# Kernel tuning notes

Measured on AMD Instinct MI355X. Metric: run time of the kernel, lower is better.

Reference implementation:

```python
import jax, jax.numpy as jnp
import numpy as np

B, C, T = 64, 128, 4096
KNOT = 4  # default knot=4 -> 6 spline knots
SIGMA = 0.2


def setup_inputs() -> dict:
    key = jax.random.key(0)
    k1, k2, k3 = jax.random.split(key, 3)
    x = jax.random.normal(k1, (B, C, T), dtype=jnp.float32)
    # yy ~ N(1.0, sigma) as in GenerateRandomCurves
    yy = 1.0 + SIGMA * jax.random.normal(k2, (B, KNOT + 2, C), dtype=jnp.float32)
    mask_rand = jax.random.uniform(k3, (B, 1, 1), dtype=jnp.float32)
    return {"x": x, "yy": yy, "mask_rand": mask_rand}


def _notaknot_matrix(n, h):
    # Moment (second-derivative) system for a not-a-knot cubic spline on a
    # uniform grid with spacing h (matches scipy.interpolate.CubicSpline default bc).
    A = np.zeros((n, n), dtype=np.float32)
    for i in range(1, n - 1):
        A[i, i - 1] = h / 6.0
        A[i, i] = 2.0 * h / 3.0
        A[i, i + 1] = h / 6.0
    # not-a-knot: third derivative continuous at x1 and x_{n-2}
    A[0, 0], A[0, 1], A[0, 2] = 1.0, -2.0, 1.0
    A[-1, -3], A[-1, -2], A[-1, -1] = 1.0, -2.0, 1.0
    return jnp.asarray(A)


def reference(x, yy, mask_rand):
    Bq, Cq, Tq = x.shape
    n = KNOT + 2
    h = (Tq - 1) / (KNOT + 1)  # uniform knot spacing; knots span [0, T-1]
    A = _notaknot_matrix(n, h)

    # Solve for spline moments M (second derivatives at knots), batched over (B, C).
    rhs_int = (yy[:, 2:, :] - 2.0 * yy[:, 1:-1, :] + yy[:, :-2, :]) / h  # (B, n-2, C)
    z = jnp.zeros((Bq, 1, Cq), yy.dtype)
    rhs = jnp.concatenate([z, rhs_int, z], axis=1)  # (B, n, C)
    M = jnp.linalg.solve(A, rhs)  # (B, n, C)

    # Evaluate the spline at t = 0..T-1 (vectorized over all batch/channel).
    tq = jnp.arange(Tq, dtype=x.dtype)
    idx = jnp.clip(jnp.floor(tq / h).astype(jnp.int32), 0, n - 2)  # (T,)
    xl = idx.astype(x.dtype) * h
    dxl = (tq - xl)[None, :, None]       # t - x_i
    dxr = (xl + h - tq)[None, :, None]   # x_{i+1} - t
    Mi, Mi1 = M[:, idx, :], M[:, idx + 1, :]      # (B, T, C)
    yi, yi1 = yy[:, idx, :], yy[:, idx + 1, :]    # (B, T, C)
    curve = ((Mi * dxr**3 + Mi1 * dxl**3) / (6.0 * h)
             + (yi / h - Mi * h / 6.0) * dxr
             + (yi1 / h - Mi1 * h / 6.0) * dxl)   # (B, T, C)

    # DistortTimesteps: cumulative sum, rescaled so the last step lands on T-1.
    tt = jnp.cumsum(curve, axis=1)
    tt = tt * (Tq - 1) / tt[:, -1:, :]  # (B, T, C)

    # Per-(batch, channel) linear interpolation back onto the regular grid.
    xp = tt.transpose(0, 2, 1).reshape(Bq * Cq, Tq)  # warped timestamps
    fp = x.reshape(Bq * Cq, Tq)                      # channel signals
    x_tw = jax.vmap(lambda a, b: jnp.interp(tq, a, b))(xp, fp)
    x_tw = x_tw.reshape(Bq, Cq, Tq)

    mask = mask_rand < 0.5  # (B,1,1): apply warp with probability p=0.5
    return jnp.where(mask, x_tw, x)
```

## Files before the change

kernel.cpp:

```cpp
#include <hip/hip_runtime.h>

#define BB 64
#define CC 128
#define TT 4096
#define NN 6
#define HH 819.0f
#define NTHR 512
#define EPT 8
#define NWAVE (NTHR / 64)
#define NROW (BB * CC)
#define NSPAN 5
#define TABBYTES ((size_t)NROW * NSPAN * 16)

typedef float f4 __attribute__((ext_vector_type(4)));

__device__ __forceinline__ void nt_store4(float* p, f4 v) {
    __builtin_nontemporal_store(v, (f4*)p);
}

__device__ __forceinline__ int padi(int j) { return j + (j >> 5); }

__device__ __forceinline__ void spline_solve(const float* __restrict__ yy,
                                             int b, int c, float* y, float* Mv)
{
    #pragma unroll
    for (int k = 0; k < NN; ++k)
        y[k] = yy[((size_t)b * NN + k) * CC + c];
    float Aug[NN][NN + 1];
    #pragma unroll
    for (int i = 0; i < NN; ++i)
        #pragma unroll
        for (int j = 0; j < NN + 1; ++j)
            Aug[i][j] = 0.0f;
    Aug[0][0] = 1.0f;  Aug[0][1] = -2.0f;  Aug[0][2] = 1.0f;
    Aug[5][3] = 1.0f;  Aug[5][4] = -2.0f;  Aug[5][5] = 1.0f;
    #pragma unroll
    for (int i = 1; i < NN - 1; ++i) {
        Aug[i][i - 1] = HH / 6.0f;
        Aug[i][i]     = 2.0f * HH / 3.0f;
        Aug[i][i + 1] = HH / 6.0f;
        Aug[i][NN]    = (y[i + 1] - 2.0f * y[i] + y[i - 1]) / HH;
    }
    #pragma unroll
    for (int k = 0; k < NN; ++k) {
        float inv = 1.0f / Aug[k][k];
        #pragma unroll
        for (int i = k + 1; i < NN; ++i) {
            float m = Aug[i][k] * inv;
            #pragma unroll
            for (int j = k; j < NN + 1; ++j)
                Aug[i][j] -= m * Aug[k][j];
        }
    }
    #pragma unroll
    for (int i = NN - 1; i >= 0; --i) {
        float s = Aug[i][NN];
        #pragma unroll
        for (int j = i + 1; j < NN; ++j)
            s -= Aug[i][j] * Mv[j];
        Mv[i] = s / Aug[i][i];
    }
}

__global__ __launch_bounds__(256) void spline_coef_kernel(
    const float* __restrict__ yy, f4* __restrict__ tab)
{
    const int row = blockIdx.x * 256 + threadIdx.x;
    const int b = row / CC;
    const int c = row % CC;
    float y[NN], Mv[NN];
    spline_solve(yy, b, c, y, Mv);
    const float invh  = 1.0f / HH;
    const float inv6h = 1.0f / (6.0f * HH);
    #pragma unroll
    for (int s = 0; s < NSPAN; ++s) {
        f4 cf;
        cf.x = y[s];
        cf.y = (y[s + 1] - y[s]) * invh - Mv[s] * (HH / 3.0f) - Mv[s + 1] * (HH / 6.0f);
        cf.z = Mv[s] * 0.5f;
        cf.w = (Mv[s + 1] - Mv[s]) * inv6h;
        tab[row * NSPAN + s] = cf;
    }
}

template <int TABLE>
__global__ __launch_bounds__(NTHR) void timewarp_kernel(
    const float* __restrict__ x,
    const float* __restrict__ yy,
    const float* __restrict__ mask_rand,
    const f4* __restrict__ tab,
    float* __restrict__ out)
{
    const int row = blockIdx.x;
    const int b   = row / CC;
    const int tid = threadIdx.x;

    const float* xrow = x + (size_t)row * TT;
    float* orow       = out + (size_t)row * TT;

    if (!(mask_rand[b] < 0.5f)) {
        const f4* xi = (const f4*)xrow;
        nt_store4(orow + 4 * tid,          xi[tid]);
        nt_store4(orow + 4 * (tid + NTHR), xi[tid + NTHR]);
        return;
    }

    __shared__ float sh_res[TT + TT / 32];
    __shared__ float sh_xx[NTHR];
    __shared__ float sh_wsum[NWAVE];

    const int t0 = tid * EPT;
    int idxA = t0 / 819;  if (idxA > 4) idxA = 4;
    int idxB = idxA + 1;  if (idxB > 4) idxB = 4;

    const f4 v0 = *(const f4*)(xrow + t0);
    const f4 v1 = *(const f4*)(xrow + t0 + 4);
    const float fpb = xrow[(t0 + EPT < TT) ? (t0 + EPT) : (TT - 1)];

    f4 cfA, cfB;
    if (TABLE) {
        cfA = tab[row * NSPAN + idxA];
        cfB = tab[row * NSPAN + idxB];
    } else {
        const int c = row % CC;
        float y[NN], Mv[NN];
        spline_solve(yy, b, c, y, Mv);
        const float invh  = 1.0f / HH;
        const float inv6h = 1.0f / (6.0f * HH);
        float MiA = Mv[0], Mi1A = Mv[1], yiA = y[0], yi1A = y[1];
        #pragma unroll
        for (int s = 1; s <= 4; ++s)
            if (idxA >= s) { MiA = Mv[s]; Mi1A = Mv[s + 1]; yiA = y[s]; yi1A = y[s + 1]; }
        float MiB = Mv[0], Mi1B = Mv[1], yiB = y[0], yi1B = y[1];
        #pragma unroll
        for (int s = 1; s <= 4; ++s)
            if (idxB >= s) { MiB = Mv[s]; Mi1B = Mv[s + 1]; yiB = y[s]; yi1B = y[s + 1]; }
        cfA.x = yiA;
        cfA.y = (yi1A - yiA) * invh - MiA * (HH / 3.0f) - Mi1A * (HH / 6.0f);
        cfA.z = MiA * 0.5f;
        cfA.w = (Mi1A - MiA) * inv6h;
        cfB.x = yiB;
        cfB.y = (yi1B - yiB) * invh - MiB * (HH / 3.0f) - Mi1B * (HH / 6.0f);
        cfB.z = MiB * 0.5f;
        cfB.w = (Mi1B - MiB) * inv6h;
    }

    float fpv[EPT];
    fpv[0] = v0.x; fpv[1] = v0.y; fpv[2] = v0.z; fpv[3] = v0.w;
    fpv[4] = v1.x; fpv[5] = v1.y; fpv[6] = v1.z; fpv[7] = v1.w;

    const float xlA = (float)idxA * HH;
    const float xlB = (float)idxB * HH;
    const float tb  = (float)((idxA + 1) * 819);

    float loc[EPT];
    float running = 0.0f;
    #pragma unroll
    for (int k = 0; k < EPT; ++k) {
        float ft = (float)(t0 + k);
        bool inB = ft >= tb;
        f4    cf = inB ? cfB : cfA;
        float xl = inB ? xlB : xlA;
        float s  = ft - xl;
        running += fmaf(s, fmaf(s, fmaf(s, cf.w, cf.z), cf.y), cf.x);
        loc[k] = running;
    }

    const int lane = tid & 63, wid = tid >> 6;
    float ws = running;
    #pragma unroll
    for (int d = 1; d < 64; d <<= 1) {
        float v = __shfl_up(ws, d, 64);
        if (lane >= d) ws += v;
    }
    if (lane == 63) sh_wsum[wid] = ws;
    __syncthreads();
    float wo = 0.0f, total = 0.0f;
    #pragma unroll
    for (int w = 0; w < NWAVE; ++w) {
        float s = sh_wsum[w];
        total += s;
        if (w < wid) wo += s;
    }
    const float offs  = wo + (ws - running);
    const float scale = 4095.0f / total;

    float xpv[EPT + 1];
    #pragma unroll
    for (int k = 0; k < EPT; ++k)
        xpv[k] = (loc[k] + offs) * scale;
    sh_xx[tid] = xpv[0];
    __syncthreads();
    xpv[EPT] = (tid < NTHR - 1) ? sh_xx[tid + 1] : 4095.0f;

    #pragma unroll
    for (int k = 0; k < EPT; ++k) {
        const int seg = t0 + k;
        if (seg < TT - 1) {
            float xa = xpv[k], xb = xpv[k + 1];
            float fa = fpv[k];
            float fb = (k < EPT - 1) ? fpv[k + 1] : fpb;
            float d  = xb - xa;
            float slope = (d > 0.0f) ? (fb - fa) * __builtin_amdgcn_rcpf(d) : 0.0f;
            float a0 = fmaf(-xa, slope, fa);
            int qlo = (int)ceilf(xa);  if (qlo < 0) qlo = 0;
            int qhi = (int)ceilf(xb);  if (qhi > TT) qhi = TT;
            for (int q = qlo; q < qhi; ++q)
                sh_res[padi(q)] = fmaf((float)q, slope, a0);
        }
    }
    if (tid == 0) {
        int q1 = (int)ceilf(xpv[0]);  if (q1 > TT) q1 = TT;
        for (int q = 0; q < q1; ++q) sh_res[padi(q)] = fpv[0];
    }
    if (tid == NTHR - 1) {
        int q0 = (int)ceilf(xpv[EPT - 1]);  if (q0 < 0) q0 = 0;
        for (int q = q0; q < TT; ++q) sh_res[padi(q)] = fpv[EPT - 1];
    }
    __syncthreads();

    #pragma unroll
    for (int kk = 0; kk < 2; ++kk) {
        int i4 = tid + NTHR * kk;
        int fb4 = 4 * i4;
        int p  = padi(fb4);
        f4 v;
        v.x = sh_res[p + 0];
        v.y = sh_res[p + 1];
        v.z = sh_res[p + 2];
        v.w = sh_res[p + 3];
        nt_store4(orow + fb4, v);
    }
}

extern "C" void kernel_launch(void* const* d_in, const int* in_sizes, int n_in,
                              void* d_out, int out_size, void* d_ws, size_t ws_size,
                              hipStream_t stream) {
    const float* x    = (const float*)d_in[0];
    const float* yy   = (const float*)d_in[1];
    const float* mask = (const float*)d_in[2];
    float* out = (float*)d_out;

    if (d_ws != nullptr && ws_size >= TABBYTES) {
        f4* tab = (f4*)d_ws;
        spline_coef_kernel<<<dim3(NROW / 256), dim3(256), 0, stream>>>(yy, tab);
        timewarp_kernel<1><<<dim3(NROW), dim3(NTHR), 0, stream>>>(x, yy, mask, tab, out);
    } else {
        timewarp_kernel<0><<<dim3(NROW), dim3(NTHR), 0, stream>>>(x, yy, mask, nullptr, out);
    }
}
```

Baseline: 235.4 us.

## Process two rows per block and replace shared-memory neighbor exchange with shuffle

```diff
diff --git a/kernel.cpp b/kernel.cpp
--- a/kernel.cpp
+++ b/kernel.cpp
@@ -11,6 +11,7 @@
 #define NROW (BB * CC)
 #define NSPAN 5
 #define TABBYTES ((size_t)NROW * NSPAN * 16)
+#define PADSZ (TT + TT / 32)
 
 typedef float f4 __attribute__((ext_vector_type(4)));
 
@@ -62,6 +63,22 @@
     }
 }
 
+__device__ __forceinline__ void horner_coefs(const float* y, const float* Mv,
+                                             f4* out5)
+{
+    const float invh  = 1.0f / HH;
+    const float inv6h = 1.0f / (6.0f * HH);
+    #pragma unroll
+    for (int s = 0; s < NSPAN; ++s) {
+        f4 cf;
+        cf.x = y[s];
+        cf.y = (y[s + 1] - y[s]) * invh - Mv[s] * (HH / 3.0f) - Mv[s + 1] * (HH / 6.0f);
+        cf.z = Mv[s] * 0.5f;
+        cf.w = (Mv[s + 1] - Mv[s]) * inv6h;
+        out5[s] = cf;
+    }
+}
+
 __global__ __launch_bounds__(256) void spline_coef_kernel(
     const float* __restrict__ yy, f4* __restrict__ tab)
 {
@@ -70,17 +87,11 @@
     const int c = row % CC;
     float y[NN], Mv[NN];
     spline_solve(yy, b, c, y, Mv);
-    const float invh  = 1.0f / HH;
-    const float inv6h = 1.0f / (6.0f * HH);
-    #pragma unroll
-    for (int s = 0; s < NSPAN; ++s) {
-        f4 cf;
-        cf.x = y[s];
-        cf.y = (y[s + 1] - y[s]) * invh - Mv[s] * (HH / 3.0f) - Mv[s + 1] * (HH / 6.0f);
-        cf.z = Mv[s] * 0.5f;
-        cf.w = (Mv[s + 1] - Mv[s]) * inv6h;
-        tab[row * NSPAN + s] = cf;
-    }
+    f4 cf[NSPAN];
+    horner_coefs(y, Mv, cf);
+    #pragma unroll
+    for (int s = 0; s < NSPAN; ++s)
+        tab[row * NSPAN + s] = cf[s];
 }
 
 template <int TABLE>
@@ -91,145 +102,189 @@
     const f4* __restrict__ tab,
     float* __restrict__ out)
 {
-    const int row = blockIdx.x;
-    const int b   = row / CC;
+    const int r0  = 2 * blockIdx.x;
+    const int r1  = r0 + 1;
+    const int b   = r0 / CC;
     const int tid = threadIdx.x;
 
-    const float* xrow = x + (size_t)row * TT;
-    float* orow       = out + (size_t)row * TT;
+    const float* xr0 = x + (size_t)r0 * TT;
+    const float* xr1 = x + (size_t)r1 * TT;
+    float* or0       = out + (size_t)r0 * TT;
+    float* or1       = out + (size_t)r1 * TT;
 
     if (!(mask_rand[b] < 0.5f)) {
-        const f4* xi = (const f4*)xrow;
-        nt_store4(orow + 4 * tid,          xi[tid]);
-        nt_store4(orow + 4 * (tid + NTHR), xi[tid + NTHR]);
+        const f4* xi0 = (const f4*)xr0;
+        const f4* xi1 = (const f4*)xr1;
+        nt_store4(or0 + 4 * tid,          xi0[tid]);
+        nt_store4(or0 + 4 * (tid + NTHR), xi0[tid + NTHR]);
+        nt_store4(or1 + 4 * tid,          xi1[tid]);
+        nt_store4(or1 + 4 * (tid + NTHR), xi1[tid + NTHR]);
         return;
     }
 
-    __shared__ float sh_res[TT + TT / 32];
-    __shared__ float sh_xx[NTHR];
-    __shared__ float sh_wsum[NWAVE];
+    __shared__ float sh_res0[PADSZ];
+    __shared__ float sh_res1[PADSZ];
+    __shared__ float sh_w0[NWAVE];
+    __shared__ float sh_w1[NWAVE];
 
     const int t0 = tid * EPT;
     int idxA = t0 / 819;  if (idxA > 4) idxA = 4;
     int idxB = idxA + 1;  if (idxB > 4) idxB = 4;
-
-    const f4 v0 = *(const f4*)(xrow + t0);
-    const f4 v1 = *(const f4*)(xrow + t0 + 4);
-    const float fpb = xrow[(t0 + EPT < TT) ? (t0 + EPT) : (TT - 1)];
-
-    f4 cfA, cfB;
-    if (TABLE) {
-        cfA = tab[row * NSPAN + idxA];
-        cfB = tab[row * NSPAN + idxB];
-    } else {
-        const int c = row % CC;
-        float y[NN], Mv[NN];
-        spline_solve(yy, b, c, y, Mv);
-        const float invh  = 1.0f / HH;
-        const float inv6h = 1.0f / (6.0f * HH);
-        float MiA = Mv[0], Mi1A = Mv[1], yiA = y[0], yi1A = y[1];
-        #pragma unroll
-        for (int s = 1; s <= 4; ++s)
-            if (idxA >= s) { MiA = Mv[s]; Mi1A = Mv[s + 1]; yiA = y[s]; yi1A = y[s + 1]; }
-        float MiB = Mv[0], Mi1B = Mv[1], yiB = y[0], yi1B = y[1];
-        #pragma unroll
-        for (int s = 1; s <= 4; ++s)
-            if (idxB >= s) { MiB = Mv[s]; Mi1B = Mv[s + 1]; yiB = y[s]; yi1B = y[s + 1]; }
-        cfA.x = yiA;
-        cfA.y = (yi1A - yiA) * invh - MiA * (HH / 3.0f) - Mi1A * (HH / 6.0f);
-        cfA.z = MiA * 0.5f;
-        cfA.w = (Mi1A - MiA) * inv6h;
-        cfB.x = yiB;
-        cfB.y = (yi1B - yiB) * invh - MiB * (HH / 3.0f) - Mi1B * (HH / 6.0f);
-        cfB.z = MiB * 0.5f;
-        cfB.w = (Mi1B - MiB) * inv6h;
-    }
-
-    float fpv[EPT];
-    fpv[0] = v0.x; fpv[1] = v0.y; fpv[2] = v0.z; fpv[3] = v0.w;
-    fpv[4] = v1.x; fpv[5] = v1.y; fpv[6] = v1.z; fpv[7] = v1.w;
-
     const float xlA = (float)idxA * HH;
     const float xlB = (float)idxB * HH;
     const float tb  = (float)((idxA + 1) * 819);
 
-    float loc[EPT];
-    float running = 0.0f;
+    const f4 a00 = *(const f4*)(xr0 + t0);
+    const f4 a01 = *(const f4*)(xr0 + t0 + 4);
+    const f4 a10 = *(const f4*)(xr1 + t0);
+    const f4 a11 = *(const f4*)(xr1 + t0 + 4);
+    const int nb8 = (t0 + EPT < TT) ? (t0 + EPT) : (TT - 1);
+    const float fpb0 = xr0[nb8];
+    const float fpb1 = xr1[nb8];
+
+    f4 cf0A, cf0B, cf1A, cf1B;
+    if (TABLE) {
+        cf0A = tab[r0 * NSPAN + idxA];  cf0B = tab[r0 * NSPAN + idxB];
+        cf1A = tab[r1 * NSPAN + idxA];  cf1B = tab[r1 * NSPAN + idxB];
+    } else {
+        float y[NN], Mv[NN];
+        f4 cf[NSPAN];
+        spline_solve(yy, b, r0 % CC, y, Mv);
+        horner_coefs(y, Mv, cf);
+        cf0A = cf[idxA];  cf0B = cf[idxB];
+        spline_solve(yy, b, r1 % CC, y, Mv);
+        horner_coefs(y, Mv, cf);
+        cf1A = cf[idxA];  cf1B = cf[idxB];
+    }
+
+    float fp0[EPT], fp1[EPT];
+    fp0[0] = a00.x; fp0[1] = a00.y; fp0[2] = a00.z; fp0[3] = a00.w;
+    fp0[4] = a01.x; fp0[5] = a01.y; fp0[6] = a01.z; fp0[7] = a01.w;
+    fp1[0] = a10.x; fp1[1] = a10.y; fp1[2] = a10.z; fp1[3] = a10.w;
+    fp1[4] = a11.x; fp1[5] = a11.y; fp1[6] = a11.z; fp1[7] = a11.w;
+
+    float lc0[EPT], lc1[EPT];
+    float run0 = 0.0f, run1 = 0.0f;
     #pragma unroll
     for (int k = 0; k < EPT; ++k) {
         float ft = (float)(t0 + k);
         bool inB = ft >= tb;
-        f4    cf = inB ? cfB : cfA;
         float xl = inB ? xlB : xlA;
         float s  = ft - xl;
-        running += fmaf(s, fmaf(s, fmaf(s, cf.w, cf.z), cf.y), cf.x);
-        loc[k] = running;
+        f4 c0 = inB ? cf0B : cf0A;
+        f4 c1 = inB ? cf1B : cf1A;
+        run0 += fmaf(s, fmaf(s, fmaf(s, c0.w, c0.z), c0.y), c0.x);
+        run1 += fmaf(s, fmaf(s, fmaf(s, c1.w, c1.z), c1.y), c1.x);
+        lc0[k] = run0;
+        lc1[k] = run1;
+    }
+    float cN0, cN1;
+    {
+        float ft = (float)(t0 + EPT);
+        bool inB = ft >= tb;
+        float xl = inB ? xlB : xlA;
+        float s  = ft - xl;
+        f4 c0 = inB ? cf0B : cf0A;
+        f4 c1 = inB ? cf1B : cf1A;
+        cN0 = fmaf(s, fmaf(s, fmaf(s, c0.w, c0.z), c0.y), c0.x);
+        cN1 = fmaf(s, fmaf(s, fmaf(s, c1.w, c1.z), c1.y), c1.x);
     }
 
     const int lane = tid & 63, wid = tid >> 6;
-    float ws = running;
+    float w0 = run0, w1 = run1;
     #pragma unroll
     for (int d = 1; d < 64; d <<= 1) {
-        float v = __shfl_up(ws, d, 64);
-        if (lane >= d) ws += v;
-    }
-    if (lane == 63) sh_wsum[wid] = ws;
+        float v0 = __shfl_up(w0, d, 64);
+        float v1 = __shfl_up(w1, d, 64);
+        if (lane >= d) { w0 += v0; w1 += v1; }
+    }
+    if (lane == 63) { sh_w0[wid] = w0; sh_w1[wid] = w1; }
     __syncthreads();
-    float wo = 0.0f, total = 0.0f;
+    float wo0 = 0.0f, tt0 = 0.0f, wo1 = 0.0f, tt1 = 0.0f;
     #pragma unroll
     for (int w = 0; w < NWAVE; ++w) {
-        float s = sh_wsum[w];
-        total += s;
-        if (w < wid) wo += s;
-    }
-    const float offs  = wo + (ws - running);
-    const float scale = 4095.0f / total;
-
-    float xpv[EPT + 1];
-    #pragma unroll
-    for (int k = 0; k < EPT; ++k)
-        xpv[k] = (loc[k] + offs) * scale;
-    sh_xx[tid] = xpv[0];
-    __syncthreads();
-    xpv[EPT] = (tid < NTHR - 1) ? sh_xx[tid + 1] : 4095.0f;
+        float s0 = sh_w0[w], s1 = sh_w1[w];
+        tt0 += s0;  tt1 += s1;
+        if (w < wid) { wo0 += s0; wo1 += s1; }
+    }
+    const float of0 = wo0 + (w0 - run0);
+    const float of1 = wo1 + (w1 - run1);
+    const float sc0 = 4095.0f / tt0;
+    const float sc1 = 4095.0f / tt1;
+
+    float xp0[EPT + 1], xp1[EPT + 1];
+    #pragma unroll
+    for (int k = 0; k < EPT; ++k) {
+        xp0[k] = (lc0[k] + of0) * sc0;
+        xp1[k] = (lc1[k] + of1) * sc1;
+    }
+    {
+        float n0 = __shfl_down(xp0[0], 1, 64);
+        float n1 = __shfl_down(xp1[0], 1, 64);
+        float l0 = ((wo0 + w0) + cN0) * sc0;
+        float l1 = ((wo1 + w1) + cN1) * sc1;
+        xp0[EPT] = (lane == 63) ? l0 : n0;
+        xp1[EPT] = (lane == 63) ? l1 : n1;
+    }
 
     #pragma unroll
     for (int k = 0; k < EPT; ++k) {
         const int seg = t0 + k;
         if (seg < TT - 1) {
-            float xa = xpv[k], xb = xpv[k + 1];
-            float fa = fpv[k];
-            float fb = (k < EPT - 1) ? fpv[k + 1] : fpb;
+            float xa = xp0[k], xb = xp0[k + 1];
+            float fa = fp0[k];
+            float fb = (k < EPT - 1) ? fp0[k + 1] : fpb0;
             float d  = xb - xa;
             float slope = (d > 0.0f) ? (fb - fa) * __builtin_amdgcn_rcpf(d) : 0.0f;
             float a0 = fmaf(-xa, slope, fa);
             int qlo = (int)ceilf(xa);  if (qlo < 0) qlo = 0;
             int qhi = (int)ceilf(xb);  if (qhi > TT) qhi = TT;
             for (int q = qlo; q < qhi; ++q)
-                sh_res[padi(q)] = fmaf((float)q, slope, a0);
+                sh_res0[padi(q)] = fmaf((float)q, slope, a0);
         }
     }
+    #pragma unroll
+    for (int k = 0; k < EPT; ++k) {
+        const int seg = t0 + k;
+        if (seg < TT - 1) {
+            float xa = xp1[k], xb = xp1[k + 1];
+            float fa = fp1[k];
+            float fb = (k < EPT - 1) ? fp1[k + 1] : fpb1;
+            float d  = xb - xa;
+            float slope = (d > 0.0f) ? (fb - fa) * __builtin_amdgcn_rcpf(d) : 0.0f;
+            float a0 = fmaf(-xa, slope, fa);
+            int qlo = (int)ceilf(xa);  if (qlo < 0) qlo = 0;
+            int qhi = (int)ceilf(xb);  if (qhi > TT) qhi = TT;
+            for (int q = qlo; q < qhi; ++q)
+                sh_res1[padi(q)] = fmaf((float)q, slope, a0);
+        }
+    }
     if (tid == 0) {
-        int q1 = (int)ceilf(xpv[0]);  if (q1 > TT) q1 = TT;
-        for (int q = 0; q < q1; ++q) sh_res[padi(q)] = fpv[0];
+        int q1 = (int)ceilf(xp0[0]);  if (q1 > TT) q1 = TT;
+        for (int q = 0; q < q1; ++q) sh_res0[padi(q)] = fp0[0];
+        q1 = (int)ceilf(xp1[0]);  if (q1 > TT) q1 = TT;
+        for (int q = 0; q < q1; ++q) sh_res1[padi(q)] = fp1[0];
     }
     if (tid == NTHR - 1) {
-        int q0 = (int)ceilf(xpv[EPT - 1]);  if (q0 < 0) q0 = 0;
-        for (int q = q0; q < TT; ++q) sh_res[padi(q)] = fpv[EPT - 1];
+        int q0 = (int)ceilf(xp0[EPT - 1]);  if (q0 < 0) q0 = 0;
+        for (int q = q0; q < TT; ++q) sh_res0[padi(q)] = fp0[EPT - 1];
+        q0 = (int)ceilf(xp1[EPT - 1]);  if (q0 < 0) q0 = 0;
+        for (int q = q0; q < TT; ++q) sh_res1[padi(q)] = fp1[EPT - 1];
     }
     __syncthreads();
 
     #pragma unroll
     for (int kk = 0; kk < 2; ++kk) {
-        int i4 = tid + NTHR * kk;
+        int i4  = tid + NTHR * kk;
         int fb4 = 4 * i4;
-        int p  = padi(fb4);
-        f4 v;
-        v.x = sh_res[p + 0];
-        v.y = sh_res[p + 1];
-        v.z = sh_res[p + 2];
-        v.w = sh_res[p + 3];
-        nt_store4(orow + fb4, v);
+        int p   = padi(fb4);
+        f4 v0, v1;
+        v0.x = sh_res0[p + 0];  v0.y = sh_res0[p + 1];
+        v0.z = sh_res0[p + 2];  v0.w = sh_res0[p + 3];
+        v1.x = sh_res1[p + 0];  v1.y = sh_res1[p + 1];
+        v1.z = sh_res1[p + 2];  v1.w = sh_res1[p + 3];
+        nt_store4(or0 + fb4, v0);
+        nt_store4(or1 + fb4, v1);
     }
 }
 
@@ -244,8 +299,8 @@
     if (d_ws != nullptr && ws_size >= TABBYTES) {
         f4* tab = (f4*)d_ws;
         spline_coef_kernel<<<dim3(NROW / 256), dim3(256), 0, stream>>>(yy, tab);
-        timewarp_kernel<1><<<dim3(NROW), dim3(NTHR), 0, stream>>>(x, yy, mask, tab, out);
+        timewarp_kernel<1><<<dim3(NROW / 2), dim3(NTHR), 0, stream>>>(x, yy, mask, tab, out);
     } else {
-        timewarp_kernel<0><<<dim3(NROW), dim3(NTHR), 0, stream>>>(x, yy, mask, nullptr, out);
-    }
-}
+        timewarp_kernel<0><<<dim3(NROW / 2), dim3(NTHR), 0, stream>>>(x, yy, mask, nullptr, out);
+    }
+}
```

New measurement: 237.4 us. No clear change (+0.9%).
